# Performance work log

Measured on AMD Instinct MI355X. Metric: run time of the kernel, lower is better.

The kernel has to match this reference:

```python
import jax, jax.numpy as jnp
import numpy as np

EMBED_DIM, HIDDEN_DIM, NUM_BINS = 1280, 256, 10

def setup_inputs() -> dict:
    key = jax.random.key(0)
    ks = jax.random.split(key, 7)
    s_in = 1.0 / np.sqrt(EMBED_DIM)
    s_h = 1.0 / np.sqrt(HIDDEN_DIM)
    return {
        "x": jax.random.normal(ks[0], (2, 384, EMBED_DIM), dtype=jnp.float32),
        "Wi": jax.random.uniform(ks[1], (EMBED_DIM, HIDDEN_DIM), jnp.float32, -s_in, s_in),
        "bi": jax.random.uniform(ks[2], (HIDDEN_DIM,), jnp.float32, -s_in, s_in),
        "Wj": jax.random.uniform(ks[3], (EMBED_DIM, HIDDEN_DIM), jnp.float32, -s_in, s_in),
        "bj": jax.random.uniform(ks[4], (HIDDEN_DIM,), jnp.float32, -s_in, s_in),
        "Wo": jax.random.uniform(ks[5], (HIDDEN_DIM, NUM_BINS), jnp.float32, -s_h, s_h),
        "bo": jax.random.uniform(ks[6], (NUM_BINS,), jnp.float32, -s_h, s_h),
    }

def reference(x, Wi, bi, Wj, bj, Wo, bo):
    # x: [B, L, D]
    xi = x @ Wi + bi              # [B, L, H]
    xj = x @ Wj + bj              # [B, L, H]
    pair = xi[:, :, None, :] * xj[:, None, :, :]   # [B, L, L, H]
    h = jax.nn.relu(pair)
    return h @ Wo + bo            # [B, L, L, num_bins]
```

## Files before the change

kernel.cpp:

```cpp
#include <hip/hip_runtime.h>

#define LSEQ 384
#define EMBED 1280
#define HID 256
#define NBINS 10
#define GM 768
#define KP 512
#define NJN (LSEQ * NBINS)
#define NKX (EMBED / 32)
#define NKP (KP / 32)

typedef __attribute__((ext_vector_type(8))) short short8;
typedef __attribute__((ext_vector_type(4))) float float4v;

__device__ __forceinline__ unsigned bfbits(float f) {
    unsigned u = __builtin_bit_cast(unsigned, f);
    return (u + 0x7fffu + ((u >> 16) & 1u)) >> 16;
}
__device__ __forceinline__ float bf2f(short s) {
    unsigned u = ((unsigned)(unsigned short)s) << 16;
    return __builtin_bit_cast(float, u);
}


__global__ __launch_bounds__(256) void k_prep(
    const float* __restrict__ x, const float* __restrict__ Wi, const float* __restrict__ Wj,
    short* __restrict__ xb_f, short* __restrict__ WT_f)
{
    __shared__ float tile[32][33];
    const int t = threadIdx.x;
    int bx = blockIdx.x;
    if (bx < 480) {
        const int cid = bx * 4 + (t >> 6);
        const int rt = cid / NKX, kc = cid - rt * NKX;
        const int lane = t & 63;
        const int row = rt * 16 + (lane & 15);
        const int k = kc * 32 + (lane >> 4) * 8;
        const float4v a = *(const float4v*)(x + (size_t)row * EMBED + k);
        const float4v b = *(const float4v*)(x + (size_t)row * EMBED + k + 4);
        short8 o;
        o[0] = (short)bfbits(a.x); o[1] = (short)bfbits(a.y);
        o[2] = (short)bfbits(a.z); o[3] = (short)bfbits(a.w);
        o[4] = (short)bfbits(b.x); o[5] = (short)bfbits(b.y);
        o[6] = (short)bfbits(b.z); o[7] = (short)bfbits(b.w);
        *(short8*)(xb_f + (size_t)cid * 512 + lane * 8) = o;
    } else {
        bx -= 480;
        const int isJ = bx >= 320 ? 1 : 0;
        if (isJ) bx -= 320;
        const int tk = bx % 40, tn = bx / 40;
        const int k0 = tk * 32, n0 = tn * 32;
        const float* __restrict__ W = isJ ? Wj : Wi;
        const int r = t >> 3, c4 = (t & 7) * 4;
        const float4v v = *(const float4v*)(W + (size_t)(k0 + r) * HID + n0 + c4);
        tile[r][c4 + 0] = v.x; tile[r][c4 + 1] = v.y;
        tile[r][c4 + 2] = v.z; tile[r][c4 + 3] = v.w;
        __syncthreads();
        const int chunkhalf = t >> 7;
        const int l = (t & 127) >> 1;
        const int hs = t & 1;
        const int n_loc = chunkhalf * 16 + (l & 15);
        const int k_loc = (l >> 4) * 8 + hs * 4;
        const int rt = isJ * 16 + tn * 2 + chunkhalf;
        unsigned d0 = bfbits(tile[k_loc + 0][n_loc]) | (bfbits(tile[k_loc + 1][n_loc]) << 16);
        unsigned d1 = bfbits(tile[k_loc + 2][n_loc]) | (bfbits(tile[k_loc + 3][n_loc]) << 16);
        unsigned* dst = (unsigned*)(WT_f + ((size_t)rt * NKX + tk) * 512 + l * 8 + hs * 4);
        dst[0] = d0; dst[1] = d1;
    }
}

__global__ __launch_bounds__(256) void k_gemm(
    const short* __restrict__ xb_f, const short* __restrict__ WT_f,
    const float* __restrict__ bi, const float* __restrict__ bj,
    short* __restrict__ A_f, short* __restrict__ Bj)
{
    __shared__ float sC[32][33];
    const int tid = threadIdx.x;
    const int lane = tid & 63, w = tid >> 6;
    const int mh = w & 1, nh = w >> 1;
    const int l15 = lane & 15, q = lane >> 4;
    const int m0 = blockIdx.x * 32, n0 = blockIdx.y * 32;
    const bool isI = (n0 < HID);

    const short* ap = xb_f + ((size_t)(blockIdx.x * 2 + mh) * NKX) * 512 + lane * 8;
    const short* bp = WT_f + ((size_t)(blockIdx.y * 2 + nh) * NKX) * 512 + lane * 8;

    float4v acc = {0.f, 0.f, 0.f, 0.f};
#pragma unroll 5
    for (int ks = 0; ks < NKX; ++ks) {
        const short8 af = *(const short8*)(ap + ks * 512);
        const short8 bf = *(const short8*)(bp + ks * 512);
        acc = __builtin_amdgcn_mfma_f32_16x16x32_bf16(af, bf, acc, 0, 0, 0);
    }

    const int nloc = nh * 16 + l15;
    const float bv = isI ? bi[n0 + nloc] : bj[n0 - HID + nloc];
#pragma unroll
    for (int r = 0; r < 4; ++r)
        sC[mh * 16 + q * 4 + r][nloc] = acc[r] + bv;
    __syncthreads();

    if (isI) {
        const int g = tid >> 7, sign = (tid >> 6) & 1, l = tid & 63;
        const int mr = g * 16 + (l & 15);
        const int kq = (l >> 4) * 8;
        short8 o;
#pragma unroll
        for (int c = 0; c < 8; ++c) {
            const float v = sC[mr][kq + c];
            o[c] = (short)bfbits(sign ? fmaxf(-v, 0.f) : fmaxf(v, 0.f));
        }
        const int rt = blockIdx.x * 2 + g;
        const int kc = (n0 >> 5) + sign * 8;
        *(short8*)(A_f + ((size_t)rt * NKP + kc) * 512 + l * 8) = o;
    } else {
        const int mr = tid >> 3;
        const int hq = (tid & 7) * 4;
        const int h = (n0 - HID) + hq;
        unsigned dp[2], dm[2];
#pragma unroll
        for (int g2 = 0; g2 < 2; ++g2) {
            const float v0 = sC[mr][hq + 2 * g2], v1 = sC[mr][hq + 2 * g2 + 1];
            dp[g2] = bfbits(fmaxf(v0, 0.f)) | (bfbits(fmaxf(v1, 0.f)) << 16);
            dm[g2] = bfbits(fmaxf(-v0, 0.f)) | (bfbits(fmaxf(-v1, 0.f)) << 16);
        }
        unsigned* basep = (unsigned*)(Bj + (size_t)(m0 + mr) * KP + h);
        unsigned* basem = (unsigned*)(Bj + (size_t)(m0 + mr) * KP + HID + h);
        basep[0] = dp[0]; basep[1] = dp[1];
        basem[0] = dm[0]; basem[1] = dm[1];
    }
}

__global__ __launch_bounds__(256) void k_pack_b(
    const short* __restrict__ Bj, const float* __restrict__ Wo, short* __restrict__ Bp_f)
{
    __shared__ float woL[HID * NBINS];
    __shared__ short bjL[3][KP];
    const int t = threadIdx.x;
    const int jt = blockIdx.x, b = blockIdx.y;
    const int j0 = (jt * 16) / NBINS;

    for (int i = t; i < HID * NBINS; i += 256) woL[i] = Wo[i];
    for (int i = t; i < 3 * 256; i += 256) {
        const int r = i >> 8, d = i & 255;
        const int jrow = j0 + r;
        const int grow = b * LSEQ + (jrow > LSEQ - 1 ? LSEQ - 1 : jrow);
        ((unsigned*)bjL[r])[d] = ((const unsigned*)(Bj + (size_t)grow * KP))[d];
    }
    __syncthreads();

    const int lane = t & 63, w = t >> 6;
    const int jn = jt * 16 + (lane & 15);
    const int j = jn / NBINS, n = jn - j * NBINS;
    const int jloc = j - j0;
    const int kq = (lane >> 4) * 8;
#pragma unroll
    for (int p = 0; p < 4; ++p) {
        const int kc = w + p * 4;
        const int kbase = kc * 32 + kq;
        short8 o;
#pragma unroll
        for (int c = 0; c < 8; ++c) {
            const int k = kbase + c;
            o[c] = (short)bfbits(bf2f(bjL[jloc][k]) * woL[(k & (HID - 1)) * NBINS + n]);
        }
        *(short8*)(Bp_f + ((size_t)(b * 240 + jt) * NKP + kc) * 512 + lane * 8) = o;
    }
}

__global__ __launch_bounds__(256) void k2_pair(
    const short* __restrict__ A_f, const short* __restrict__ Bp_f,
    const float* __restrict__ bo, float* __restrict__ out)
{
    const int tid = threadIdx.x;
    const int lane = tid & 63, w = tid >> 6;
    const int iw = w & 1, jw = w >> 1;
    const int l15 = lane & 15, q = lane >> 4;
    const int b = blockIdx.z;
    const int i0 = blockIdx.x * 64, jn0 = blockIdx.y * 64;

    const short* ap = A_f + ((size_t)(b * 24 + (i0 >> 4) + iw * 2) * NKP) * 512 + lane * 8;
    const short* bp = Bp_f + ((size_t)(b * 240 + (jn0 >> 4) + jw * 2) * NKP) * 512 + lane * 8;

    float4v acc[2][2];
#pragma unroll
    for (int ia = 0; ia < 2; ++ia)
#pragma unroll
        for (int jb = 0; jb < 2; ++jb) acc[ia][jb] = (float4v){0.f, 0.f, 0.f, 0.f};

#pragma unroll 2
    for (int ks = 0; ks < NKP; ++ks) {
        const short8 af0 = *(const short8*)(ap + ks * 512);
        const short8 af1 = *(const short8*)(ap + (NKP + ks) * 512);
        const short8 bf0 = *(const short8*)(bp + ks * 512);
        const short8 bf1 = *(const short8*)(bp + (NKP + ks) * 512);
        acc[0][0] = __builtin_amdgcn_mfma_f32_16x16x32_bf16(af0, bf0, acc[0][0], 0, 0, 0);
        acc[0][1] = __builtin_amdgcn_mfma_f32_16x16x32_bf16(af0, bf1, acc[0][1], 0, 0, 0);
        acc[1][0] = __builtin_amdgcn_mfma_f32_16x16x32_bf16(af1, bf0, acc[1][0], 0, 0, 0);
        acc[1][1] = __builtin_amdgcn_mfma_f32_16x16x32_bf16(af1, bf1, acc[1][1], 0, 0, 0);
    }

#pragma unroll
    for (int jb = 0; jb < 2; ++jb) {
        const int jn = jn0 + jw * 32 + jb * 16 + l15;
        const int n = jn - (jn / NBINS) * NBINS;
        const float bv = bo[n];
#pragma unroll
        for (int ia = 0; ia < 2; ++ia) {
            const int i = i0 + iw * 32 + ia * 16 + q * 4;
            float* orow = out + ((size_t)(b * LSEQ + i) * NJN) + jn;
#pragma unroll
            for (int r = 0; r < 4; ++r)
                orow[(size_t)r * NJN] = acc[ia][jb][r] + bv;
        }
    }
}

extern "C" void kernel_launch(void* const* d_in, const int* in_sizes, int n_in,
                              void* d_out, int out_size, void* d_ws, size_t ws_size,
                              hipStream_t stream)
{
    const float* x  = (const float*)d_in[0];
    const float* Wi = (const float*)d_in[1];
    const float* bi = (const float*)d_in[2];
    const float* Wj = (const float*)d_in[3];
    const float* bj = (const float*)d_in[4];
    const float* Wo = (const float*)d_in[5];
    const float* bo = (const float*)d_in[6];
    float* out = (float*)d_out;

    char* p = (char*)d_ws;
    short* xb_f = (short*)p;  p += (size_t)48 * NKX * 512 * 2;
    short* WT_f = (short*)p;  p += (size_t)32 * NKX * 512 * 2;
    short* A_f  = (short*)p;  p += (size_t)48 * NKP * 512 * 2;
    short* Bj   = (short*)p;  p += (size_t)GM * KP * 2;
    short* Bp_f = (short*)p;

    k_prep<<<1120, 256, 0, stream>>>(x, Wi, Wj, xb_f, WT_f);
    k_gemm<<<dim3(GM / 32, 512 / 32), 256, 0, stream>>>(xb_f, WT_f, bi, bj, A_f, Bj);
    k_pack_b<<<dim3(240, 2), 256, 0, stream>>>(Bj, Wo, Bp_f);
    k2_pair<<<dim3(LSEQ / 64, NJN / 64, 2), 256, 0, stream>>>(A_f, Bp_f, bo, out);
}
```

Before: 99.06 us.

## Fuse Wo-scaled B packing into GEMM epilogue and widen pair-kernel j tile

The pack_b kernel is removed. The projection GEMM's j-half epilogue now multiplies the relu'd positive and negative parts by Wo, which it stages in shared memory, and writes the MFMA-fragment layout for the pair GEMM directly. This drops one launch and the round trip through the intermediate Bj buffer. Separately, the pair kernel gives each wave 4 B fragments instead of 2, so each block covers 128 jn columns and reuses A loads more, at the cost of more accumulator registers and half as many blocks.

```diff
diff --git a/kernel.cpp b/kernel.cpp
--- a/kernel.cpp
+++ b/kernel.cpp
@@ -16,10 +16,6 @@
 __device__ __forceinline__ unsigned bfbits(float f) {
     unsigned u = __builtin_bit_cast(unsigned, f);
     return (u + 0x7fffu + ((u >> 16) & 1u)) >> 16;
-}
-__device__ __forceinline__ float bf2f(short s) {
-    unsigned u = ((unsigned)(unsigned short)s) << 16;
-    return __builtin_bit_cast(float, u);
 }
 
 
@@ -69,12 +65,13 @@
     }
 }
 
-__global__ __launch_bounds__(256) void k_gemm(
+__global__ __launch_bounds__(256) void k_gemm_pack(
     const short* __restrict__ xb_f, const short* __restrict__ WT_f,
-    const float* __restrict__ bi, const float* __restrict__ bj,
-    short* __restrict__ A_f, short* __restrict__ Bj)
+    const float* __restrict__ bi, const float* __restrict__ bj, const float* __restrict__ Wo,
+    short* __restrict__ A_f, short* __restrict__ Bp_f)
 {
     __shared__ float sC[32][33];
+    __shared__ float woS[32 * NBINS];
     const int tid = threadIdx.x;
     const int lane = tid & 63, w = tid >> 6;
     const int mh = w & 1, nh = w >> 1;
@@ -82,6 +79,10 @@
     const int m0 = blockIdx.x * 32, n0 = blockIdx.y * 32;
     const bool isI = (n0 < HID);
 
+    if (!isI) {
+        for (int i = tid; i < 32 * NBINS; i += 256) woS[i] = Wo[(n0 - HID) * NBINS + i];
+    }
+
     const short* ap = xb_f + ((size_t)(blockIdx.x * 2 + mh) * NKX) * 512 + lane * 8;
     const short* bp = WT_f + ((size_t)(blockIdx.y * 2 + nh) * NKX) * 512 + lane * 8;
 
@@ -114,57 +115,32 @@
         const int kc = (n0 >> 5) + sign * 8;
         *(short8*)(A_f + ((size_t)rt * NKP + kc) * 512 + l * 8) = o;
     } else {
-        const int mr = tid >> 3;
-        const int hq = (tid & 7) * 4;
-        const int h = (n0 - HID) + hq;
-        unsigned dp[2], dm[2];
-#pragma unroll
-        for (int g2 = 0; g2 < 2; ++g2) {
-            const float v0 = sC[mr][hq + 2 * g2], v1 = sC[mr][hq + 2 * g2 + 1];
-            dp[g2] = bfbits(fmaxf(v0, 0.f)) | (bfbits(fmaxf(v1, 0.f)) << 16);
-            dm[g2] = bfbits(fmaxf(-v0, 0.f)) | (bfbits(fmaxf(-v1, 0.f)) << 16);
-        }
-        unsigned* basep = (unsigned*)(Bj + (size_t)(m0 + mr) * KP + h);
-        unsigned* basem = (unsigned*)(Bj + (size_t)(m0 + mr) * KP + HID + h);
-        basep[0] = dp[0]; basep[1] = dp[1];
-        basem[0] = dm[0]; basem[1] = dm[1];
-    }
-}
-
-__global__ __launch_bounds__(256) void k_pack_b(
-    const short* __restrict__ Bj, const float* __restrict__ Wo, short* __restrict__ Bp_f)
-{
-    __shared__ float woL[HID * NBINS];
-    __shared__ short bjL[3][KP];
-    const int t = threadIdx.x;
-    const int jt = blockIdx.x, b = blockIdx.y;
-    const int j0 = (jt * 16) / NBINS;
-
-    for (int i = t; i < HID * NBINS; i += 256) woL[i] = Wo[i];
-    for (int i = t; i < 3 * 256; i += 256) {
-        const int r = i >> 8, d = i & 255;
-        const int jrow = j0 + r;
-        const int grow = b * LSEQ + (jrow > LSEQ - 1 ? LSEQ - 1 : jrow);
-        ((unsigned*)bjL[r])[d] = ((const unsigned*)(Bj + (size_t)grow * KP))[d];
-    }
-    __syncthreads();
-
-    const int lane = t & 63, w = t >> 6;
-    const int jn = jt * 16 + (lane & 15);
-    const int j = jn / NBINS, n = jn - j * NBINS;
-    const int jloc = j - j0;
-    const int kq = (lane >> 4) * 8;
-#pragma unroll
-    for (int p = 0; p < 4; ++p) {
-        const int kc = w + p * 4;
-        const int kbase = kc * 32 + kq;
-        short8 o;
-#pragma unroll
-        for (int c = 0; c < 8; ++c) {
-            const int k = kbase + c;
-            o[c] = (short)bfbits(bf2f(bjL[jloc][k]) * woL[(k & (HID - 1)) * NBINS + n]);
-        }
-        *(short8*)(Bp_f + ((size_t)(b * 240 + jt) * NKP + kc) * 512 + lane * 8) = o;
+        const int h0 = n0 - HID;
+        const int bb = m0 >= LSEQ ? 1 : 0;
+        const int jloc0 = m0 - bb * LSEQ;
+        const int rt0 = (jloc0 * NBINS) >> 4;
+        const int l = tid & 63;
+        const int c0 = tid >> 6;
+        const int ll15 = l & 15, e8 = (l >> 4) * 8;
+#pragma unroll
+        for (int s = 0; s < 10; ++s) {
+            const int c = s * 4 + c0;
+            const int sgn = c & 1, rtl = c >> 1;
+            const int jn = (rt0 + rtl) * 16 + ll15;
+            const int j = (jn * 6554) >> 16;
+            const int n = jn - j * NBINS;
+            const int jl = j - jloc0;
+            short8 o;
+#pragma unroll
+            for (int e = 0; e < 8; ++e) {
+                const int hc = e8 + e;
+                const float v = sC[jl][hc];
+                const float p = sgn ? fmaxf(-v, 0.f) : fmaxf(v, 0.f);
+                o[e] = (short)bfbits(p * woS[hc * NBINS + n]);
+            }
+            const int kc = (h0 >> 5) + sgn * 8;
+            *(short8*)(Bp_f + ((size_t)(bb * 240 + rt0 + rtl) * NKP + kc) * 512 + l * 8) = o;
+        }
     }
 }
 
@@ -177,33 +153,37 @@
     const int iw = w & 1, jw = w >> 1;
     const int l15 = lane & 15, q = lane >> 4;
     const int b = blockIdx.z;
-    const int i0 = blockIdx.x * 64, jn0 = blockIdx.y * 64;
+    const int i0 = blockIdx.x * 64, jn0 = blockIdx.y * 128;
 
     const short* ap = A_f + ((size_t)(b * 24 + (i0 >> 4) + iw * 2) * NKP) * 512 + lane * 8;
-    const short* bp = Bp_f + ((size_t)(b * 240 + (jn0 >> 4) + jw * 2) * NKP) * 512 + lane * 8;
-
-    float4v acc[2][2];
+    const short* bp = Bp_f + ((size_t)(b * 240 + (jn0 >> 4) + jw * 4) * NKP) * 512 + lane * 8;
+
+    float4v acc[2][4];
 #pragma unroll
     for (int ia = 0; ia < 2; ++ia)
 #pragma unroll
-        for (int jb = 0; jb < 2; ++jb) acc[ia][jb] = (float4v){0.f, 0.f, 0.f, 0.f};
+        for (int jb = 0; jb < 4; ++jb) acc[ia][jb] = (float4v){0.f, 0.f, 0.f, 0.f};
 
 #pragma unroll 2
     for (int ks = 0; ks < NKP; ++ks) {
         const short8 af0 = *(const short8*)(ap + ks * 512);
         const short8 af1 = *(const short8*)(ap + (NKP + ks) * 512);
-        const short8 bf0 = *(const short8*)(bp + ks * 512);
-        const short8 bf1 = *(const short8*)(bp + (NKP + ks) * 512);
-        acc[0][0] = __builtin_amdgcn_mfma_f32_16x16x32_bf16(af0, bf0, acc[0][0], 0, 0, 0);
-        acc[0][1] = __builtin_amdgcn_mfma_f32_16x16x32_bf16(af0, bf1, acc[0][1], 0, 0, 0);
-        acc[1][0] = __builtin_amdgcn_mfma_f32_16x16x32_bf16(af1, bf0, acc[1][0], 0, 0, 0);
-        acc[1][1] = __builtin_amdgcn_mfma_f32_16x16x32_bf16(af1, bf1, acc[1][1], 0, 0, 0);
-    }
-
-#pragma unroll
-    for (int jb = 0; jb < 2; ++jb) {
-        const int jn = jn0 + jw * 32 + jb * 16 + l15;
-        const int n = jn - (jn / NBINS) * NBINS;
+        short8 bf[4];
+#pragma unroll
+        for (int jb = 0; jb < 4; ++jb)
+            bf[jb] = *(const short8*)(bp + ((size_t)jb * NKP + ks) * 512);
+#pragma unroll
+        for (int jb = 0; jb < 4; ++jb) {
+            acc[0][jb] = __builtin_amdgcn_mfma_f32_16x16x32_bf16(af0, bf[jb], acc[0][jb], 0, 0, 0);
+            acc[1][jb] = __builtin_amdgcn_mfma_f32_16x16x32_bf16(af1, bf[jb], acc[1][jb], 0, 0, 0);
+        }
+    }
+
+#pragma unroll
+    for (int jb = 0; jb < 4; ++jb) {
+        const int jn = jn0 + jw * 64 + jb * 16 + l15;
+        const int jq = (jn * 6554) >> 16;
+        const int n = jn - jq * NBINS;
         const float bv = bo[n];
 #pragma unroll
         for (int ia = 0; ia < 2; ++ia) {
@@ -233,11 +213,9 @@
     short* xb_f = (short*)p;  p += (size_t)48 * NKX * 512 * 2;
     short* WT_f = (short*)p;  p += (size_t)32 * NKX * 512 * 2;
     short* A_f  = (short*)p;  p += (size_t)48 * NKP * 512 * 2;
-    short* Bj   = (short*)p;  p += (size_t)GM * KP * 2;
     short* Bp_f = (short*)p;
 
     k_prep<<<1120, 256, 0, stream>>>(x, Wi, Wj, xb_f, WT_f);
-    k_gemm<<<dim3(GM / 32, 512 / 32), 256, 0, stream>>>(xb_f, WT_f, bi, bj, A_f, Bj);
-    k_pack_b<<<dim3(240, 2), 256, 0, stream>>>(Bj, Wo, Bp_f);
-    k2_pair<<<dim3(LSEQ / 64, NJN / 64, 2), 256, 0, stream>>>(A_f, Bp_f, bo, out);
-}
+    k_gemm_pack<<<dim3(GM / 32, 512 / 32), 256, 0, stream>>>(xb_f, WT_f, bi, bj, Wo, A_f, Bp_f);
+    k2_pair<<<dim3(LSEQ / 64, NJN / 128, 2), 256, 0, stream>>>(A_f, Bp_f, bo, out);
+}
```

Result: faster. 95.24 us (-3.9%).
